# Kernel optimization log

Measured on AMD Instinct MI355X. Metric: run time of the kernel, lower is better.

Reference implementation:

```python
import jax, jax.numpy as jnp
import numpy as np

B, N, E = 16, 1024, 32768
D_IN, HID, HEADS, OUT = 33, 32, 4, 8  # OUT = d_mid // heads
EPS = 1e-5
NEG_SLOPE = 0.2  # PyG GATConv default leaky_relu slope


def layer_norm(x, g, b):
    m = x.mean(-1, keepdims=True)
    v = ((x - m) ** 2).mean(-1, keepdims=True)
    return (x - m) / jnp.sqrt(v + EPS) * g + b


def gat_conv(x, src, dst, W, a_src, a_dst, bias):
    # x: [N, F_in]; W: [F_in, HEADS*OUT]; a_src/a_dst: [HEADS, OUT]
    n = x.shape[0]
    xp = (x @ W).reshape(n, HEADS, OUT)                 # [N, H, D]
    al_s = (xp * a_src).sum(-1)                          # [N, H]
    al_d = (xp * a_dst).sum(-1)                          # [N, H]
    e = jax.nn.leaky_relu(al_s[src] + al_d[dst], NEG_SLOPE)  # [E, H]
    # softmax over incoming edges per target node (PyG: softmax over edge_index[1])
    m = jax.ops.segment_max(e, dst, num_segments=n)
    ex = jnp.exp(e - m[dst])
    s = jax.ops.segment_sum(ex, dst, num_segments=n)
    alpha = ex / s[dst]                                  # [E, H]
    out = jax.ops.segment_sum(xp[src] * alpha[:, :, None], dst, num_segments=n)
    return out.reshape(n, HEADS * OUT) + bias, alpha


def setup_inputs() -> dict:
    key = jax.random.key(0)
    ks = jax.random.split(key, 16)
    inp = {
        "H": jax.random.normal(ks[0], (B, N, D_IN), jnp.float32),
        "edge_index": jax.random.randint(ks[1], (2, E), 0, N, dtype=jnp.int64),
        # ObsEmbedding params
        "W1_e": jax.random.normal(ks[2], (D_IN, HID), jnp.float32) * 0.1,
        "b1_e": jnp.zeros((HID,), jnp.float32),
        "W2_e": jax.random.normal(ks[3], (HID, HID), jnp.float32) * 0.1,
        "b2_e": jnp.zeros((HID,), jnp.float32),
        "ln_e_g": jnp.ones((HID,), jnp.float32),
        "ln_e_b": jnp.zeros((HID,), jnp.float32),
        # GAT1 params
        "W_g1": jax.random.normal(ks[4], (HID, HEADS * OUT), jnp.float32) * 0.1,
        "as_g1": jax.random.normal(ks[5], (HEADS, OUT), jnp.float32) * 0.1,
        "ad_g1": jax.random.normal(ks[6], (HEADS, OUT), jnp.float32) * 0.1,
        "bi_g1": jnp.zeros((HEADS * OUT,), jnp.float32),
        # GAT2 params
        "W_g2": jax.random.normal(ks[7], (HEADS * OUT, HEADS * OUT), jnp.float32) * 0.1,
        "as_g2": jax.random.normal(ks[8], (HEADS, OUT), jnp.float32) * 0.1,
        "ad_g2": jax.random.normal(ks[9], (HEADS, OUT), jnp.float32) * 0.1,
        "bi_g2": jnp.zeros((HEADS * OUT,), jnp.float32),
        # output LayerNorm
        "ln_o_g": jnp.ones((HEADS * OUT,), jnp.float32),
        "ln_o_b": jnp.zeros((HEADS * OUT,), jnp.float32),
    }
    return inp


def reference(H, edge_index, W1_e, b1_e, W2_e, b2_e, ln_e_g, ln_e_b,
              W_g1, as_g1, ad_g1, bi_g1, W_g2, as_g2, ad_g2, bi_g2,
              ln_o_g, ln_o_b):
    src, dst = edge_index[0], edge_index[1]

    # ObsEmbedding: Linear->ReLU->Linear->ReLU->LayerNorm (batched, dense)
    x = jax.nn.relu(H @ W1_e + b1_e)
    x = jax.nn.relu(x @ W2_e + b2_e)
    x = layer_norm(x, ln_e_g, ln_e_b)          # [B, N, 32]

    def per_graph(xb):
        h1, _ = gat_conv(xb, src, dst, W_g1, as_g1, ad_g1, bi_g1)
        h1 = jax.nn.relu(h1)
        h2, alpha2 = gat_conv(h1, src, dst, W_g2, as_g2, ad_g2, bi_g2)
        h_out = layer_norm(h1 + h2, ln_o_g, ln_o_b)
        return h_out, alpha2

    h_out, alpha2 = jax.vmap(per_graph)(x)      # [B, N, 32], [B, E, HEADS]

    # scatter edge attention into dense [B, HEADS, N, N] at [src, dst]
    alpha_t = jnp.transpose(alpha2, (0, 2, 1))  # [B, HEADS, E]
    A = jnp.zeros((B, HEADS, N, N), jnp.float32).at[:, :, src, dst].set(alpha_t)
    return h_out, A
```

## Files before the change

### kernel.cpp

```cpp
#include <hip/hip_runtime.h>
#include <hip/hip_bf16.h>

#define BB 16
#define NN 1024
#define EE 32768
#define D_IN 33
#define HID 32
#define HEADS 4
#define OUTD 8
#define FF 32
#define EPSL 1e-5f
#define SLOPE 0.2f

__device__ __forceinline__ float red32(float v) {
    v += __shfl_xor(v, 1);
    v += __shfl_xor(v, 2);
    v += __shfl_xor(v, 4);
    v += __shfl_xor(v, 8);
    v += __shfl_xor(v, 16);
    return v;
}
__device__ __forceinline__ float red8(float v) {
    v += __shfl_xor(v, 1);
    v += __shfl_xor(v, 2);
    v += __shfl_xor(v, 4);
    return v;
}

__global__ __launch_bounds__(256) void k_init(int* __restrict__ deg,
                                              int* __restrict__ deg2) {
    int i = threadIdx.x;
    for (int k = i; k < NN; k += 256) { deg[k] = 0; deg2[k] = 0; }
}

__global__ __launch_bounds__(256) void k_count(const int* __restrict__ ei,
                                               int* __restrict__ deg,
                                               int* __restrict__ deg2) {
    int e = blockIdx.x * 256 + threadIdx.x;
    if (e < EE) {
        atomicAdd(&deg[ei[EE + e]], 1);
        atomicAdd(&deg2[ei[e]], 1);
    }
}

__global__ __launch_bounds__(1024) void k_scan(
    const int* __restrict__ deg, int* __restrict__ off, int* __restrict__ cur,
    const int* __restrict__ deg2, int* __restrict__ off2, int* __restrict__ cur2) {
    __shared__ int tmp[NN];
    int t = threadIdx.x;
    tmp[t] = deg[t];
    __syncthreads();
    for (int s = 1; s < NN; s <<= 1) {
        int v = (t >= s) ? tmp[t - s] : 0;
        __syncthreads();
        tmp[t] += v;
        __syncthreads();
    }
    off[t + 1] = tmp[t];
    if (t == 0) off[0] = 0;
    cur[t] = (t == 0) ? 0 : tmp[t - 1];
    __syncthreads();
    tmp[t] = deg2[t];
    __syncthreads();
    for (int s = 1; s < NN; s <<= 1) {
        int v = (t >= s) ? tmp[t - s] : 0;
        __syncthreads();
        tmp[t] += v;
        __syncthreads();
    }
    off2[t + 1] = tmp[t];
    if (t == 0) off2[0] = 0;
    cur2[t] = (t == 0) ? 0 : tmp[t - 1];
}

__global__ __launch_bounds__(256) void k_fill(const int* __restrict__ ei,
                                              int* __restrict__ cur,
                                              int* __restrict__ csr_src,
                                              int* __restrict__ cur2,
                                              int* __restrict__ out_dst,
                                              int* __restrict__ csr_opos) {
    int e = blockIdx.x * 256 + threadIdx.x;
    if (e < EE) {
        int s = ei[e], d = ei[EE + e];
        int p = atomicAdd(&cur[d], 1);
        csr_src[p] = s;
        int p2 = atomicAdd(&cur2[s], 1);
        out_dst[p2] = d;
        csr_opos[p] = p2;
    }
}

__global__ __launch_bounds__(256) void k_embed(
    const float* __restrict__ Hm, const float* __restrict__ W1,
    const float* __restrict__ b1, const float* __restrict__ W2,
    const float* __restrict__ b2, const float* __restrict__ lng,
    const float* __restrict__ lnb, const float* __restrict__ Wg1,
    const float* __restrict__ as1, const float* __restrict__ ad1,
    float* __restrict__ xp1, float* __restrict__ als1, float* __restrict__ ald1) {
    __shared__ float sW1[D_IN * 32];
    __shared__ float sW2[32 * 32];
    __shared__ float sWg[32 * 32];
    __shared__ float sb1[32], sb2[32], sg[32], sbt[32], sas[32], sad[32];
    __shared__ float sh[8][34];
    __shared__ float sx[8][33];
    int tid = threadIdx.x;
    for (int i = tid; i < D_IN * 32; i += 256) sW1[i] = W1[i];
    for (int i = tid; i < 1024; i += 256) { sW2[i] = W2[i]; sWg[i] = Wg1[i]; }
    if (tid < 32) {
        sb1[tid] = b1[tid]; sb2[tid] = b2[tid];
        sg[tid] = lng[tid]; sbt[tid] = lnb[tid];
        sas[tid] = as1[tid]; sad[tid] = ad1[tid];
    }
    int g = tid >> 5, j = tid & 31;
    int idx = blockIdx.x * 8 + g;
    __syncthreads();
    int base = idx * D_IN;
    for (int i = j; i < D_IN; i += 32) sh[g][i] = Hm[base + i];
    __syncthreads();
    float acc = sb1[j];
#pragma unroll
    for (int i = 0; i < D_IN; i++) acc += sh[g][i] * sW1[i * 32 + j];
    float x1 = fmaxf(acc, 0.f);
    sx[g][j] = x1;
    __syncthreads();
    acc = sb2[j];
#pragma unroll
    for (int i = 0; i < 32; i++) acc += sx[g][i] * sW2[i * 32 + j];
    float x2 = fmaxf(acc, 0.f);
    float mean = red32(x2) * (1.f / 32.f);
    float d0 = x2 - mean;
    float var = red32(d0 * d0) * (1.f / 32.f);
    float xn = d0 * rsqrtf(var + EPSL) * sg[j] + sbt[j];
    __syncthreads();
    sx[g][j] = xn;
    __syncthreads();
    acc = 0.f;
#pragma unroll
    for (int i = 0; i < 32; i++) acc += sx[g][i] * sWg[i * 32 + j];
    xp1[idx * 32 + j] = acc;
    float ps = red8(acc * sas[j]);
    float pd = red8(acc * sad[j]);
    if ((j & 7) == 0) {
        als1[idx * 4 + (j >> 3)] = ps;
        ald1[idx * 4 + (j >> 3)] = pd;
    }
}

__global__ __launch_bounds__(256) void k_gat1(
    const int* __restrict__ off, const int* __restrict__ csr_src,
    const float* __restrict__ xp1, const float* __restrict__ als1,
    const float* __restrict__ ald1, const float* __restrict__ bi1,
    const float* __restrict__ Wg2, const float* __restrict__ as2,
    const float* __restrict__ ad2, float* __restrict__ h1,
    float* __restrict__ xp2, float* __restrict__ als2, float* __restrict__ ald2) {
    __shared__ float sW[1024];
    __shared__ float sb[32], sas[32], sad[32];
    __shared__ float sx[8][33];
    __shared__ float salp[8][32];
    __shared__ int   ssrc[8][8];
    int tid = threadIdx.x;
    for (int i = tid; i < 1024; i += 256) sW[i] = Wg2[i];
    if (tid < 32) { sb[tid] = bi1[tid]; sas[tid] = as2[tid]; sad[tid] = ad2[tid]; }
    __syncthreads();
    int g = tid >> 5, j = tid & 31, h = j >> 3, t8 = j & 7;
    int idx = blockIdx.x * 8 + g;
    int b = idx >> 10, n = idx & 1023;
    int beg = off[n], end = off[n + 1];
    float aldh = ald1[idx * 4 + h];
    const float* alsb = als1 + b * NN * 4;
    float se = 0.f;
    for (int k = beg + t8; k < end; k += 8) {
        int s = csr_src[k];
        float av = alsb[s * 4 + h] + aldh;
        av = av > 0.f ? av : SLOPE * av;
        se += __expf(av);
    }
    se = red8(se);
    float inv = se > 0.f ? 1.f / se : 0.f;
    const float* xpb = xp1 + b * NN * 32;
    float acc = 0.f;
    for (int kb = beg; kb < end; kb += 8) {
        int k = kb + t8;
        float al = 0.f; int s = 0;
        if (k < end) {
            s = csr_src[k];
            float av = alsb[s * 4 + h] + aldh;
            av = av > 0.f ? av : SLOPE * av;
            al = __expf(av) * inv;
        }
        salp[g][j] = al;
        if (h == 0) ssrc[g][t8] = s;
        __builtin_amdgcn_wave_barrier();
#pragma unroll
        for (int t = 0; t < 8; t++)
            acc += salp[g][(h << 3) + t] * xpb[ssrc[g][t] * 32 + j];
        __builtin_amdgcn_wave_barrier();
    }
    float hv = fmaxf(acc + sb[j], 0.f);
    h1[idx * 32 + j] = hv;
    sx[g][j] = hv;
    __syncthreads();
    float x2 = 0.f;
#pragma unroll
    for (int i = 0; i < 32; i++) x2 += sx[g][i] * sW[i * 32 + j];
    xp2[idx * 32 + j] = x2;
    float ps = red8(x2 * sas[j]);
    float pd = red8(x2 * sad[j]);
    if ((j & 7) == 0) { als2[idx * 4 + h] = ps; ald2[idx * 4 + h] = pd; }
}

__global__ __launch_bounds__(256) void k_gat2(
    const int* __restrict__ off, const int* __restrict__ csr_src,
    const int* __restrict__ csr_opos, const float* __restrict__ xp2,
    const float* __restrict__ als2, const float* __restrict__ ald2,
    const float* __restrict__ h1, const float* __restrict__ bi2,
    const float* __restrict__ lng, const float* __restrict__ lnb,
    float* __restrict__ outH, float* __restrict__ alphaE) {
    __shared__ float sb[32], sg[32], sbt[32];
    __shared__ float salp[8][32];
    __shared__ int   ssrc[8][8];
    int tid = threadIdx.x;
    if (tid < 32) { sb[tid] = bi2[tid]; sg[tid] = lng[tid]; sbt[tid] = lnb[tid]; }
    __syncthreads();
    int g = tid >> 5, j = tid & 31, h = j >> 3, t8 = j & 7;
    int idx = blockIdx.x * 8 + g;
    int b = idx >> 10, n = idx & 1023;
    int beg = off[n], end = off[n + 1];
    float aldh = ald2[idx * 4 + h];
    const float* alsb = als2 + b * NN * 4;
    float se = 0.f;
    for (int k = beg + t8; k < end; k += 8) {
        int s = csr_src[k];
        float av = alsb[s * 4 + h] + aldh;
        av = av > 0.f ? av : SLOPE * av;
        se += __expf(av);
    }
    se = red8(se);
    float inv = se > 0.f ? 1.f / se : 0.f;
    const float* xpb = xp2 + b * NN * 32;
    float* aEb = alphaE + ((size_t)b * 4 + h) * EE;
    float acc = 0.f;
    for (int kb = beg; kb < end; kb += 8) {
        int k = kb + t8;
        float al = 0.f; int s = 0;
        if (k < end) {
            s = csr_src[k];
            float av = alsb[s * 4 + h] + aldh;
            av = av > 0.f ? av : SLOPE * av;
            al = __expf(av) * inv;
            aEb[csr_opos[k]] = al;
        }
        salp[g][j] = al;
        if (h == 0) ssrc[g][t8] = s;
        __builtin_amdgcn_wave_barrier();
#pragma unroll
        for (int t = 0; t < 8; t++)
            acc += salp[g][(h << 3) + t] * xpb[ssrc[g][t] * 32 + j];
        __builtin_amdgcn_wave_barrier();
    }
    float y = h1[idx * 32 + j] + acc + sb[j];
    float mean = red32(y) * (1.f / 32.f);
    float d0 = y - mean;
    float var = red32(d0 * d0) * (1.f / 32.f);
    outH[idx * 32 + j] = d0 * rsqrtf(var + EPSL) * sg[j] + sbt[j];
}

#define ROWS_PER_BLOCK 4
__global__ __launch_bounds__(256) void k_rowA(
    const int* __restrict__ off2, const int* __restrict__ out_dst,
    const float* __restrict__ alphaE, float* __restrict__ A) {
    __shared__ float sRow[ROWS_PER_BLOCK][NN];
    int wid = threadIdx.x >> 6, lane = threadIdx.x & 63;
    int r = blockIdx.x * ROWS_PER_BLOCK + wid;
    int bh = r >> 10, src = r & 1023;
    float4* row4 = (float4*)&sRow[wid][0];
    float4 z = make_float4(0.f, 0.f, 0.f, 0.f);
#pragma unroll
    for (int i = 0; i < 4; i++) row4[i * 64 + lane] = z;
    __builtin_amdgcn_wave_barrier();
    int beg = off2[src], end = off2[src + 1];
    const float* aE = alphaE + (size_t)bh * EE;
    for (int p = beg + lane; p < end; p += 64)
        sRow[wid][out_dst[p]] = aE[p];
    __builtin_amdgcn_wave_barrier();
    float4* o4 = (float4*)(A + (size_t)bh * (NN * NN) + (size_t)src * NN);
#pragma unroll
    for (int i = 0; i < 4; i++) o4[i * 64 + lane] = row4[i * 64 + lane];
}

extern "C" void kernel_launch(void* const* d_in, const int* in_sizes, int n_in,
                              void* d_out, int out_size, void* d_ws, size_t ws_size,
                              hipStream_t stream) {
    const float* Hm  = (const float*)d_in[0];
    const int*   ei  = (const int*)d_in[1];
    const float* W1  = (const float*)d_in[2];
    const float* b1  = (const float*)d_in[3];
    const float* W2  = (const float*)d_in[4];
    const float* b2  = (const float*)d_in[5];
    const float* lneg = (const float*)d_in[6];
    const float* lneb = (const float*)d_in[7];
    const float* Wg1 = (const float*)d_in[8];
    const float* as1 = (const float*)d_in[9];
    const float* ad1 = (const float*)d_in[10];
    const float* bi1 = (const float*)d_in[11];
    const float* Wg2 = (const float*)d_in[12];
    const float* as2 = (const float*)d_in[13];
    const float* ad2 = (const float*)d_in[14];
    const float* bi2 = (const float*)d_in[15];
    const float* lnog = (const float*)d_in[16];
    const float* lnob = (const float*)d_in[17];

    float* outH = (float*)d_out;
    float* A    = outH + BB * NN * FF;

    int* deg      = (int*)d_ws;
    int* off      = deg + 1024;
    int* cur      = off + 1028;
    int* deg2     = cur + 1024;
    int* off2     = deg2 + 1024;
    int* cur2     = off2 + 1028;
    int* csr_src  = cur2 + 1024;
    int* csr_opos = csr_src + EE;
    int* out_dst  = csr_opos + EE;
    float* fb     = (float*)(out_dst + EE);
    float* xp1    = fb;
    float* als1   = xp1 + BB * NN * FF;
    float* ald1   = als1 + BB * NN * 4;
    float* h1     = ald1 + BB * NN * 4;
    float* xp2    = h1 + BB * NN * FF;
    float* als2   = xp2 + BB * NN * FF;
    float* ald2   = als2 + BB * NN * 4;
    float* alphaE = ald2 + BB * NN * 4;

    hipLaunchKernelGGL(k_init, dim3(1), dim3(256), 0, stream, deg, deg2);
    hipLaunchKernelGGL(k_count, dim3(EE / 256), dim3(256), 0, stream, ei, deg, deg2);
    hipLaunchKernelGGL(k_scan, dim3(1), dim3(1024), 0, stream,
                       deg, off, cur, deg2, off2, cur2);
    hipLaunchKernelGGL(k_fill, dim3(EE / 256), dim3(256), 0, stream,
                       ei, cur, csr_src, cur2, out_dst, csr_opos);
    hipLaunchKernelGGL(k_embed, dim3(BB * NN / 8), dim3(256), 0, stream,
                       Hm, W1, b1, W2, b2, lneg, lneb, Wg1, as1, ad1,
                       xp1, als1, ald1);
    hipLaunchKernelGGL(k_gat1, dim3(BB * NN / 8), dim3(256), 0, stream,
                       off, csr_src, xp1, als1, ald1, bi1, Wg2, as2, ad2,
                       h1, xp2, als2, ald2);
    hipLaunchKernelGGL(k_gat2, dim3(BB * NN / 8), dim3(256), 0, stream,
                       off, csr_src, csr_opos, xp2, als2, ald2, h1, bi2, lnog, lnob,
                       outH, alphaE);
    hipLaunchKernelGGL(k_rowA, dim3(BB * HEADS * NN / ROWS_PER_BLOCK), dim3(256),
                       0, stream, off2, out_dst, alphaE, A);
}
```

Baseline: 396.3 us.

## Fuse CSR build into embed kernel, single-pass softmax, recompute alpha in row scatter

Merges the degree count and prefix scan into one extra block of the embedding kernel, which removes three small launches. The GAT aggregation now runs as a single pass over edges, accumulating the softmax denominator and normalizing at the end, so the separate sum loop goes away. Instead of writing per-edge alphas through csr_opos, gat2 stores only the per-node inverse denominators, and the A-row kernel recomputes each alpha from als2/ald2. The exchange is extra exp work in the row kernel and one serial block doing the CSR scan alongside the embedding, which reduces the edge-sized global traffic. Without max subtraction, the exponentials could overflow for large logits, though the original code already skipped the max.

```diff
diff --git a/kernel.cpp b/kernel.cpp
--- a/kernel.cpp
+++ b/kernel.cpp
@@ -26,59 +26,132 @@
     v += __shfl_xor(v, 4);
     return v;
 }
-
-__global__ __launch_bounds__(256) void k_init(int* __restrict__ deg,
-                                              int* __restrict__ deg2) {
-    int i = threadIdx.x;
-    for (int k = i; k < NN; k += 256) { deg[k] = 0; deg2[k] = 0; }
-}
-
-__global__ __launch_bounds__(256) void k_count(const int* __restrict__ ei,
-                                               int* __restrict__ deg,
-                                               int* __restrict__ deg2) {
-    int e = blockIdx.x * 256 + threadIdx.x;
-    if (e < EE) {
-        atomicAdd(&deg[ei[EE + e]], 1);
-        atomicAdd(&deg2[ei[e]], 1);
-    }
-}
-
-__global__ __launch_bounds__(1024) void k_scan(
-    const int* __restrict__ deg, int* __restrict__ off, int* __restrict__ cur,
-    const int* __restrict__ deg2, int* __restrict__ off2, int* __restrict__ cur2) {
-    __shared__ int tmp[NN];
-    int t = threadIdx.x;
-    tmp[t] = deg[t];
+__device__ __forceinline__ void wb() { __builtin_amdgcn_wave_barrier(); }
+
+struct EmbedS {
+    float sW1[D_IN * 32];
+    float sW2[1024];
+    float sWg[1024];
+    float sb1[32], sb2[32], sg[32], sbt[32], sas[32], sad[32];
+    float sh[8][34];
+    float sx[8][33];
+};
+struct CsrS {
+    int hh[1024];
+    int hh2[1024];
+    int sp[256];
+};
+
+__global__ __launch_bounds__(256) void k_embed_csr(
+    const float* __restrict__ Hm, const float* __restrict__ W1,
+    const float* __restrict__ b1, const float* __restrict__ W2,
+    const float* __restrict__ b2, const float* __restrict__ lng,
+    const float* __restrict__ lnb, const float* __restrict__ Wg1,
+    const float* __restrict__ as1, const float* __restrict__ ad1,
+    float* __restrict__ xp1, float* __restrict__ als1, float* __restrict__ ald1,
+    const int* __restrict__ ei, int* __restrict__ off, int* __restrict__ cur,
+    int* __restrict__ off2, int* __restrict__ cur2) {
+    __shared__ union { EmbedS e; CsrS c; } sm;
+    int tid = threadIdx.x;
+    if (blockIdx.x == 2048) {
+        int t = tid;
+#pragma unroll
+        for (int i = 0; i < 4; i++) { sm.c.hh[t + 256 * i] = 0; sm.c.hh2[t + 256 * i] = 0; }
+        __syncthreads();
+        for (int e = t; e < EE; e += 256) {
+            int s = ei[e], d = ei[EE + e];
+            atomicAdd(&sm.c.hh[d], 1);
+            atomicAdd(&sm.c.hh2[s], 1);
+        }
+        __syncthreads();
+        {
+            int a0 = sm.c.hh[4 * t], a1 = sm.c.hh[4 * t + 1];
+            int a2 = sm.c.hh[4 * t + 2], a3 = sm.c.hh[4 * t + 3];
+            int s0 = a0, s01 = a0 + a1, s012 = s01 + a2, tot = s012 + a3;
+            sm.c.sp[t] = tot;
+            __syncthreads();
+            for (int st = 1; st < 256; st <<= 1) {
+                int u = (t >= st) ? sm.c.sp[t - st] : 0;
+                __syncthreads();
+                sm.c.sp[t] += u;
+                __syncthreads();
+            }
+            int ex = t ? sm.c.sp[t - 1] : 0;
+            off[4 * t + 1] = ex + s0; off[4 * t + 2] = ex + s01;
+            off[4 * t + 3] = ex + s012; off[4 * t + 4] = ex + tot;
+            if (t == 0) off[0] = 0;
+            cur[4 * t] = ex; cur[4 * t + 1] = ex + s0;
+            cur[4 * t + 2] = ex + s01; cur[4 * t + 3] = ex + s012;
+            __syncthreads();
+        }
+        {
+            int a0 = sm.c.hh2[4 * t], a1 = sm.c.hh2[4 * t + 1];
+            int a2 = sm.c.hh2[4 * t + 2], a3 = sm.c.hh2[4 * t + 3];
+            int s0 = a0, s01 = a0 + a1, s012 = s01 + a2, tot = s012 + a3;
+            sm.c.sp[t] = tot;
+            __syncthreads();
+            for (int st = 1; st < 256; st <<= 1) {
+                int u = (t >= st) ? sm.c.sp[t - st] : 0;
+                __syncthreads();
+                sm.c.sp[t] += u;
+                __syncthreads();
+            }
+            int ex = t ? sm.c.sp[t - 1] : 0;
+            off2[4 * t + 1] = ex + s0; off2[4 * t + 2] = ex + s01;
+            off2[4 * t + 3] = ex + s012; off2[4 * t + 4] = ex + tot;
+            if (t == 0) off2[0] = 0;
+            cur2[4 * t] = ex; cur2[4 * t + 1] = ex + s0;
+            cur2[4 * t + 2] = ex + s01; cur2[4 * t + 3] = ex + s012;
+        }
+        return;
+    }
+    for (int i = tid; i < D_IN * 32; i += 256) sm.e.sW1[i] = W1[i];
+    for (int i = tid; i < 1024; i += 256) { sm.e.sW2[i] = W2[i]; sm.e.sWg[i] = Wg1[i]; }
+    if (tid < 32) {
+        sm.e.sb1[tid] = b1[tid]; sm.e.sb2[tid] = b2[tid];
+        sm.e.sg[tid] = lng[tid]; sm.e.sbt[tid] = lnb[tid];
+        sm.e.sas[tid] = as1[tid]; sm.e.sad[tid] = ad1[tid];
+    }
+    int g = tid >> 5, j = tid & 31;
+    int idx = blockIdx.x * 8 + g;
     __syncthreads();
-    for (int s = 1; s < NN; s <<= 1) {
-        int v = (t >= s) ? tmp[t - s] : 0;
-        __syncthreads();
-        tmp[t] += v;
-        __syncthreads();
-    }
-    off[t + 1] = tmp[t];
-    if (t == 0) off[0] = 0;
-    cur[t] = (t == 0) ? 0 : tmp[t - 1];
-    __syncthreads();
-    tmp[t] = deg2[t];
-    __syncthreads();
-    for (int s = 1; s < NN; s <<= 1) {
-        int v = (t >= s) ? tmp[t - s] : 0;
-        __syncthreads();
-        tmp[t] += v;
-        __syncthreads();
-    }
-    off2[t + 1] = tmp[t];
-    if (t == 0) off2[0] = 0;
-    cur2[t] = (t == 0) ? 0 : tmp[t - 1];
+    int base = idx * D_IN;
+    for (int i = j; i < D_IN; i += 32) sm.e.sh[g][i] = Hm[base + i];
+    wb();
+    float acc = sm.e.sb1[j];
+#pragma unroll
+    for (int i = 0; i < D_IN; i++) acc += sm.e.sh[g][i] * sm.e.sW1[i * 32 + j];
+    float x1 = fmaxf(acc, 0.f);
+    sm.e.sx[g][j] = x1;
+    wb();
+    acc = sm.e.sb2[j];
+#pragma unroll
+    for (int i = 0; i < 32; i++) acc += sm.e.sx[g][i] * sm.e.sW2[i * 32 + j];
+    float x2 = fmaxf(acc, 0.f);
+    float mean = red32(x2) * (1.f / 32.f);
+    float d0 = x2 - mean;
+    float var = red32(d0 * d0) * (1.f / 32.f);
+    float xn = d0 * rsqrtf(var + EPSL) * sm.e.sg[j] + sm.e.sbt[j];
+    wb();
+    sm.e.sx[g][j] = xn;
+    wb();
+    acc = 0.f;
+#pragma unroll
+    for (int i = 0; i < 32; i++) acc += sm.e.sx[g][i] * sm.e.sWg[i * 32 + j];
+    xp1[idx * 32 + j] = acc;
+    float ps = red8(acc * sm.e.sas[j]);
+    float pd = red8(acc * sm.e.sad[j]);
+    if ((j & 7) == 0) {
+        als1[idx * 4 + (j >> 3)] = ps;
+        ald1[idx * 4 + (j >> 3)] = pd;
+    }
 }
 
 __global__ __launch_bounds__(256) void k_fill(const int* __restrict__ ei,
                                               int* __restrict__ cur,
                                               int* __restrict__ csr_src,
                                               int* __restrict__ cur2,
-                                              int* __restrict__ out_dst,
-                                              int* __restrict__ csr_opos) {
+                                              int* __restrict__ out_dst) {
     int e = blockIdx.x * 256 + threadIdx.x;
     if (e < EE) {
         int s = ei[e], d = ei[EE + e];
@@ -86,63 +159,6 @@
         csr_src[p] = s;
         int p2 = atomicAdd(&cur2[s], 1);
         out_dst[p2] = d;
-        csr_opos[p] = p2;
-    }
-}
-
-__global__ __launch_bounds__(256) void k_embed(
-    const float* __restrict__ Hm, const float* __restrict__ W1,
-    const float* __restrict__ b1, const float* __restrict__ W2,
-    const float* __restrict__ b2, const float* __restrict__ lng,
-    const float* __restrict__ lnb, const float* __restrict__ Wg1,
-    const float* __restrict__ as1, const float* __restrict__ ad1,
-    float* __restrict__ xp1, float* __restrict__ als1, float* __restrict__ ald1) {
-    __shared__ float sW1[D_IN * 32];
-    __shared__ float sW2[32 * 32];
-    __shared__ float sWg[32 * 32];
-    __shared__ float sb1[32], sb2[32], sg[32], sbt[32], sas[32], sad[32];
-    __shared__ float sh[8][34];
-    __shared__ float sx[8][33];
-    int tid = threadIdx.x;
-    for (int i = tid; i < D_IN * 32; i += 256) sW1[i] = W1[i];
-    for (int i = tid; i < 1024; i += 256) { sW2[i] = W2[i]; sWg[i] = Wg1[i]; }
-    if (tid < 32) {
-        sb1[tid] = b1[tid]; sb2[tid] = b2[tid];
-        sg[tid] = lng[tid]; sbt[tid] = lnb[tid];
-        sas[tid] = as1[tid]; sad[tid] = ad1[tid];
-    }
-    int g = tid >> 5, j = tid & 31;
-    int idx = blockIdx.x * 8 + g;
-    __syncthreads();
-    int base = idx * D_IN;
-    for (int i = j; i < D_IN; i += 32) sh[g][i] = Hm[base + i];
-    __syncthreads();
-    float acc = sb1[j];
-#pragma unroll
-    for (int i = 0; i < D_IN; i++) acc += sh[g][i] * sW1[i * 32 + j];
-    float x1 = fmaxf(acc, 0.f);
-    sx[g][j] = x1;
-    __syncthreads();
-    acc = sb2[j];
-#pragma unroll
-    for (int i = 0; i < 32; i++) acc += sx[g][i] * sW2[i * 32 + j];
-    float x2 = fmaxf(acc, 0.f);
-    float mean = red32(x2) * (1.f / 32.f);
-    float d0 = x2 - mean;
-    float var = red32(d0 * d0) * (1.f / 32.f);
-    float xn = d0 * rsqrtf(var + EPSL) * sg[j] + sbt[j];
-    __syncthreads();
-    sx[g][j] = xn;
-    __syncthreads();
-    acc = 0.f;
-#pragma unroll
-    for (int i = 0; i < 32; i++) acc += sx[g][i] * sWg[i * 32 + j];
-    xp1[idx * 32 + j] = acc;
-    float ps = red8(acc * sas[j]);
-    float pd = red8(acc * sad[j]);
-    if ((j & 7) == 0) {
-        als1[idx * 4 + (j >> 3)] = ps;
-        ald1[idx * 4 + (j >> 3)] = pd;
     }
 }
 
@@ -168,17 +184,8 @@
     int beg = off[n], end = off[n + 1];
     float aldh = ald1[idx * 4 + h];
     const float* alsb = als1 + b * NN * 4;
-    float se = 0.f;
-    for (int k = beg + t8; k < end; k += 8) {
-        int s = csr_src[k];
-        float av = alsb[s * 4 + h] + aldh;
-        av = av > 0.f ? av : SLOPE * av;
-        se += __expf(av);
-    }
-    se = red8(se);
-    float inv = se > 0.f ? 1.f / se : 0.f;
     const float* xpb = xp1 + b * NN * 32;
-    float acc = 0.f;
+    float se = 0.f, acc = 0.f;
     for (int kb = beg; kb < end; kb += 8) {
         int k = kb + t8;
         float al = 0.f; int s = 0;
@@ -186,36 +193,43 @@
             s = csr_src[k];
             float av = alsb[s * 4 + h] + aldh;
             av = av > 0.f ? av : SLOPE * av;
-            al = __expf(av) * inv;
-        }
+            al = __expf(av);
+        }
+        se += al;
         salp[g][j] = al;
         if (h == 0) ssrc[g][t8] = s;
-        __builtin_amdgcn_wave_barrier();
+        wb();
 #pragma unroll
         for (int t = 0; t < 8; t++)
             acc += salp[g][(h << 3) + t] * xpb[ssrc[g][t] * 32 + j];
-        __builtin_amdgcn_wave_barrier();
-    }
+        wb();
+    }
+    se = red8(se);
+    float inv = se > 0.f ? 1.f / se : 0.f;
+    acc *= inv;
     float hv = fmaxf(acc + sb[j], 0.f);
     h1[idx * 32 + j] = hv;
     sx[g][j] = hv;
-    __syncthreads();
+    wb();
     float x2 = 0.f;
 #pragma unroll
     for (int i = 0; i < 32; i++) x2 += sx[g][i] * sW[i * 32 + j];
     xp2[idx * 32 + j] = x2;
     float ps = red8(x2 * sas[j]);
     float pd = red8(x2 * sad[j]);
-    if ((j & 7) == 0) { als2[idx * 4 + h] = ps; ald2[idx * 4 + h] = pd; }
+    if (t8 == 0) {
+        als2[idx * 4 + h] = ps;
+        ald2[((b * 4 + h) << 10) + n] = pd;
+    }
 }
 
 __global__ __launch_bounds__(256) void k_gat2(
     const int* __restrict__ off, const int* __restrict__ csr_src,
-    const int* __restrict__ csr_opos, const float* __restrict__ xp2,
-    const float* __restrict__ als2, const float* __restrict__ ald2,
-    const float* __restrict__ h1, const float* __restrict__ bi2,
-    const float* __restrict__ lng, const float* __restrict__ lnb,
-    float* __restrict__ outH, float* __restrict__ alphaE) {
+    const float* __restrict__ xp2, const float* __restrict__ als2,
+    const float* __restrict__ ald2, const float* __restrict__ h1,
+    const float* __restrict__ bi2, const float* __restrict__ lng,
+    const float* __restrict__ lnb, float* __restrict__ outH,
+    float* __restrict__ dinv) {
     __shared__ float sb[32], sg[32], sbt[32];
     __shared__ float salp[8][32];
     __shared__ int   ssrc[8][8];
@@ -226,20 +240,10 @@
     int idx = blockIdx.x * 8 + g;
     int b = idx >> 10, n = idx & 1023;
     int beg = off[n], end = off[n + 1];
-    float aldh = ald2[idx * 4 + h];
+    float aldh = ald2[((b * 4 + h) << 10) + n];
     const float* alsb = als2 + b * NN * 4;
-    float se = 0.f;
-    for (int k = beg + t8; k < end; k += 8) {
-        int s = csr_src[k];
-        float av = alsb[s * 4 + h] + aldh;
-        av = av > 0.f ? av : SLOPE * av;
-        se += __expf(av);
-    }
-    se = red8(se);
-    float inv = se > 0.f ? 1.f / se : 0.f;
     const float* xpb = xp2 + b * NN * 32;
-    float* aEb = alphaE + ((size_t)b * 4 + h) * EE;
-    float acc = 0.f;
+    float se = 0.f, acc = 0.f;
     for (int kb = beg; kb < end; kb += 8) {
         int k = kb + t8;
         float al = 0.f; int s = 0;
@@ -247,17 +251,21 @@
             s = csr_src[k];
             float av = alsb[s * 4 + h] + aldh;
             av = av > 0.f ? av : SLOPE * av;
-            al = __expf(av) * inv;
-            aEb[csr_opos[k]] = al;
-        }
+            al = __expf(av);
+        }
+        se += al;
         salp[g][j] = al;
         if (h == 0) ssrc[g][t8] = s;
-        __builtin_amdgcn_wave_barrier();
+        wb();
 #pragma unroll
         for (int t = 0; t < 8; t++)
             acc += salp[g][(h << 3) + t] * xpb[ssrc[g][t] * 32 + j];
-        __builtin_amdgcn_wave_barrier();
-    }
+        wb();
+    }
+    se = red8(se);
+    float inv = se > 0.f ? 1.f / se : 0.f;
+    if (t8 == 0) dinv[((b * 4 + h) << 10) + n] = inv;
+    acc *= inv;
     float y = h1[idx * 32 + j] + acc + sb[j];
     float mean = red32(y) * (1.f / 32.f);
     float d0 = y - mean;
@@ -268,21 +276,29 @@
 #define ROWS_PER_BLOCK 4
 __global__ __launch_bounds__(256) void k_rowA(
     const int* __restrict__ off2, const int* __restrict__ out_dst,
-    const float* __restrict__ alphaE, float* __restrict__ A) {
+    const float* __restrict__ als2, const float* __restrict__ ald2,
+    const float* __restrict__ dinv, float* __restrict__ A) {
     __shared__ float sRow[ROWS_PER_BLOCK][NN];
     int wid = threadIdx.x >> 6, lane = threadIdx.x & 63;
     int r = blockIdx.x * ROWS_PER_BLOCK + wid;
     int bh = r >> 10, src = r & 1023;
+    int b = bh >> 2, h = bh & 3;
+    float sS = als2[((b << 10) + src) * 4 + h];
+    const float* aldv = ald2 + ((size_t)bh << 10);
+    const float* dinvv = dinv + ((size_t)bh << 10);
     float4* row4 = (float4*)&sRow[wid][0];
     float4 z = make_float4(0.f, 0.f, 0.f, 0.f);
 #pragma unroll
     for (int i = 0; i < 4; i++) row4[i * 64 + lane] = z;
-    __builtin_amdgcn_wave_barrier();
+    wb();
     int beg = off2[src], end = off2[src + 1];
-    const float* aE = alphaE + (size_t)bh * EE;
-    for (int p = beg + lane; p < end; p += 64)
-        sRow[wid][out_dst[p]] = aE[p];
-    __builtin_amdgcn_wave_barrier();
+    for (int p = beg + lane; p < end; p += 64) {
+        int d = out_dst[p];
+        float lg = sS + aldv[d];
+        lg = lg > 0.f ? lg : SLOPE * lg;
+        sRow[wid][d] = __expf(lg) * dinvv[d];
+    }
+    wb();
     float4* o4 = (float4*)(A + (size_t)bh * (NN * NN) + (size_t)src * NN);
 #pragma unroll
     for (int i = 0; i < 4; i++) o4[i * 64 + lane] = row4[i * 64 + lane];
@@ -313,15 +329,12 @@
     float* outH = (float*)d_out;
     float* A    = outH + BB * NN * FF;
 
-    int* deg      = (int*)d_ws;
-    int* off      = deg + 1024;
+    int* off      = (int*)d_ws;
     int* cur      = off + 1028;
-    int* deg2     = cur + 1024;
-    int* off2     = deg2 + 1024;
+    int* off2     = cur + 1024;
     int* cur2     = off2 + 1028;
     int* csr_src  = cur2 + 1024;
-    int* csr_opos = csr_src + EE;
-    int* out_dst  = csr_opos + EE;
+    int* out_dst  = csr_src + EE;
     float* fb     = (float*)(out_dst + EE);
     float* xp1    = fb;
     float* als1   = xp1 + BB * NN * FF;
@@ -330,23 +343,19 @@
     float* xp2    = h1 + BB * NN * FF;
     float* als2   = xp2 + BB * NN * FF;
     float* ald2   = als2 + BB * NN * 4;
-    float* alphaE = ald2 + BB * NN * 4;
-
-    hipLaunchKernelGGL(k_init, dim3(1), dim3(256), 0, stream, deg, deg2);
-    hipLaunchKernelGGL(k_count, dim3(EE / 256), dim3(256), 0, stream, ei, deg, deg2);
-    hipLaunchKernelGGL(k_scan, dim3(1), dim3(1024), 0, stream,
-                       deg, off, cur, deg2, off2, cur2);
+    float* dinv   = ald2 + BB * NN * 4;
+
+    hipLaunchKernelGGL(k_embed_csr, dim3(BB * NN / 8 + 1), dim3(256), 0, stream,
+                       Hm, W1, b1, W2, b2, lneg, lneb, Wg1, as1, ad1,
+                       xp1, als1, ald1, ei, off, cur, off2, cur2);
     hipLaunchKernelGGL(k_fill, dim3(EE / 256), dim3(256), 0, stream,
-                       ei, cur, csr_src, cur2, out_dst, csr_opos);
-    hipLaunchKernelGGL(k_embed, dim3(BB * NN / 8), dim3(256), 0, stream,
-                       Hm, W1, b1, W2, b2, lneg, lneb, Wg1, as1, ad1,
-                       xp1, als1, ald1);
+                       ei, cur, csr_src, cur2, out_dst);
     hipLaunchKernelGGL(k_gat1, dim3(BB * NN / 8), dim3(256), 0, stream,
                        off, csr_src, xp1, als1, ald1, bi1, Wg2, as2, ad2,
                        h1, xp2, als2, ald2);
     hipLaunchKernelGGL(k_gat2, dim3(BB * NN / 8), dim3(256), 0, stream,
-                       off, csr_src, csr_opos, xp2, als2, ald2, h1, bi2, lnog, lnob,
-                       outH, alphaE);
+                       off, csr_src, xp2, als2, ald2, h1, bi2, lnog, lnob,
+                       outH, dinv);
     hipLaunchKernelGGL(k_rowA, dim3(BB * HEADS * NN / ROWS_PER_BLOCK), dim3(256),
-                       0, stream, off2, out_dst, alphaE, A);
-}
+                       0, stream, off2, out_dst, als2, ald2, dinv, A);
+}
```

Measured after the change: 417.6 us. +5.4%, slower.
